# Kernel tuning notes

Measured on AMD Instinct MI355X. Metric: run time of the kernel, lower is better.

Reference implementation:

```python
import jax, jax.numpy as jnp
import numpy as np

B, T, V, E, H1, H2 = 256, 512, 50000, 300, 50, 10


def _lstm(xs, mask, W_ih, W_hh, b, hidden):
    """Masked LSTM over time-major xs [T,B,D]. mask [T,B,1]: True = valid step.
    Matches PyTorch gate order (i,f,g,o). Padded steps freeze (h,c), which is
    equivalent to pack_padded_sequence semantics (final hidden = state at last
    valid timestep)."""
    Bn = xs.shape[1]
    h0 = jnp.zeros((Bn, hidden), xs.dtype)
    c0 = jnp.zeros((Bn, hidden), xs.dtype)

    def step(carry, inp):
        h, c = carry
        x_t, m_t = inp
        g = x_t @ W_ih.T + h @ W_hh.T + b  # [B, 4H]
        i, f, gg, o = jnp.split(g, 4, axis=-1)
        c_new = jax.nn.sigmoid(f) * c + jax.nn.sigmoid(i) * jnp.tanh(gg)
        h_new = jax.nn.sigmoid(o) * jnp.tanh(c_new)
        h = jnp.where(m_t, h_new, h)
        c = jnp.where(m_t, c_new, c)
        return (h, c), h

    (hT, _), hs = jax.lax.scan(step, (h0, c0), (xs, mask))
    return hs, hT


def setup_inputs() -> dict:
    key = jax.random.key(0)
    ks = jax.random.split(key, 12)
    x = jax.random.randint(ks[0], (B, T), 0, V, dtype=jnp.int64)
    lengths = jax.random.randint(ks[1], (B,), 1, T + 1, dtype=jnp.int64)
    emb = jax.random.normal(ks[2], (V, E), dtype=jnp.float32)
    s1 = 1.0 / np.sqrt(H1)
    s2 = 1.0 / np.sqrt(H2)
    return {
        "x": x,
        "lengths": lengths,
        "emb": emb,
        "W_ih1": jax.random.uniform(ks[3], (4 * H1, E), jnp.float32, -s1, s1),
        "W_hh1": jax.random.uniform(ks[4], (4 * H1, H1), jnp.float32, -s1, s1),
        "b1": jax.random.uniform(ks[5], (4 * H1,), jnp.float32, -s1, s1),
        "W_ih2": jax.random.uniform(ks[6], (4 * H2, H1), jnp.float32, -s2, s2),
        "W_hh2": jax.random.uniform(ks[7], (4 * H2, H2), jnp.float32, -s2, s2),
        "b2": jax.random.uniform(ks[8], (4 * H2,), jnp.float32, -s2, s2),
        "fc1_w": jax.random.uniform(ks[9], (10, H2), jnp.float32, -s2, s2),
        "fc1_b": jnp.zeros((10,), jnp.float32),
        "fc2_w": jax.random.uniform(ks[10], (1, 10), jnp.float32, -s2, s2),
        "fc2_b": jnp.zeros((1,), jnp.float32),
    }


def reference(x, lengths, emb, W_ih1, W_hh1, b1, W_ih2, W_hh2, b2,
              fc1_w, fc1_b, fc2_w, fc2_b):
    e = emb[x]                                   # [B,T,E]
    xs = jnp.transpose(e, (1, 0, 2))             # time-major [T,B,E]
    mask = (jnp.arange(T)[:, None] < lengths[None, :])[..., None]  # [T,B,1]
    hs1, _ = _lstm(xs, mask, W_ih1, W_hh1, b1, H1)   # [T,B,50]
    _, h2 = _lstm(hs1, mask, W_ih2, W_hh2, b2, H2)   # final hidden [B,10]
    # dropout layers are identity in eval mode
    z = jax.nn.relu(h2 @ fc1_w.T + fc1_b)
    return z @ fc2_w.T + fc2_b                   # [B,1]
```

## Files before the change

### kernel.cpp

```cpp
#include <hip/hip_runtime.h>
#include <hip/hip_bf16.h>

#define BB 256
#define TT 512
#define EE 300
#define G4 200
#define NPAD 208
#define KP 1216
#define KC 64
#define KPD (KP/2)
#define KCD (KC/2)
#define NCH 19
#define NT 13
#define BOFF 8192
#define BUFB 34816

typedef __attribute__((ext_vector_type(8))) short short8v;
typedef __attribute__((ext_vector_type(4))) float float4v;
typedef __attribute__((ext_vector_type(4))) unsigned int uint4v;


__device__ __forceinline__ float sigm(float x) {
    return __builtin_amdgcn_rcpf(1.f + __builtin_amdgcn_exp2f(-1.442695040888963f * x));
}
__device__ __forceinline__ float tanh_(float x) {
    float t = __builtin_amdgcn_exp2f(2.885390081777927f * x);
    return 1.f - 2.f * __builtin_amdgcn_rcpf(t + 1.f);
}
template <int C>
__device__ __forceinline__ float qb(float v) {
    return __int_as_float(__builtin_amdgcn_mov_dpp(__float_as_int(v), C, 0xF, 0xF, true));
}

__device__ __forceinline__ uint2 bfsplit(float a) {
    unsigned u = __float_as_uint(a);
    unsigned rh = (u + 0x7FFFu + ((u >> 16) & 1u)) & 0xFFFF0000u;
    float l = a - __uint_as_float(rh);
    unsigned v = __float_as_uint(l);
    unsigned rl = (v + 0x7FFFu + ((v >> 16) & 1u)) >> 16;
    return make_uint2(rh >> 16, rl);
}

__global__ void wtrans_kernel(const float* __restrict__ W, const float* __restrict__ b1,
                              unsigned* __restrict__ Btg, float* __restrict__ b1p) {
    int e = blockIdx.x;
    int j = threadIdx.x;
    if (j >= NPAD) return;
    float w = 0.f;
    if (j < G4) w = W[((j & 3) * 50 + (j >> 2)) * EE + e];
    uint2 s = bfsplit(w);
    *(uint2*)(Btg + (size_t)j * KPD + 2 * e) =
        make_uint2(s.x | (s.x << 16), s.y | (s.y << 16));
    if (e == 0) b1p[j] = (j < G4) ? b1[(j & 3) * 50 + (j >> 2)] : 0.f;
}

__global__ __launch_bounds__(256, 2) void proj_kernel(
    const int* __restrict__ x, const int* __restrict__ lengths,
    const float* __restrict__ emb, const unsigned* __restrict__ Btg,
    const float* __restrict__ b1p, float* __restrict__ G1, int b0)
{
    const int b  = b0 + blockIdx.y;
    const int t0 = blockIdx.x * 64;
    const int len = lengths[b];
    if (t0 >= len) return;

    const int tid  = threadIdx.x;
    const int wv   = tid >> 6;
    const int lane = tid & 63;

    __shared__ __align__(16) char lds[2 * BUFB];

    const int arow = tid >> 2;
    const int ag   = tid & 3;
    const float* er = emb + (size_t)x[b * TT + t0 + arow] * EE;

    float4v acc[NT] = {};

    auto stageB = [&](int c, int q) {
        char* base = lds + q * BUFB + BOFF;
        #pragma unroll
        for (int rr = 0; rr < 7; ++rr) {
            if (rr < 6 || tid < 128) {
                int g   = rr * 256 + tid;
                int row = g >> 3, sl = g & 7;
                const unsigned* src = Btg + (size_t)row * KPD + c * KCD
                                      + ((sl ^ (row & 7)) << 2);
                char* dst = base + (rr * 256 + (tid & ~63)) * 16;
                __builtin_amdgcn_global_load_lds(
                    (const __attribute__((address_space(1))) void*)src,
                    (__attribute__((address_space(3))) void*)dst, 16, 0, 0);
            }
        }
    };
    auto loadA = [&](int cc) -> float4 {
        int k0 = cc * 16 + ag * 4;
        if (k0 < EE) return *(const float4*)(er + k0);
        return make_float4(0.f, 0.f, 0.f, 0.f);
    };
    auto writeA = [&](int q, float4 av) {
        uint2 s0 = bfsplit(av.x), s1 = bfsplit(av.y);
        uint2 s2 = bfsplit(av.z), s3 = bfsplit(av.w);
        unsigned p0 = s0.x | (s0.y << 16), p1 = s1.x | (s1.y << 16);
        unsigned p2 = s2.x | (s2.y << 16), p3 = s3.x | (s3.y << 16);
        char* base = lds + q * BUFB + (arow << 7);
        int r7 = arow & 7;
        *(uint4v*)(base + ((( 2 * ag    ) ^ r7) << 4)) = uint4v{p0, p0, p1, p1};
        *(uint4v*)(base + (((2 * ag + 1) ^ r7) << 4)) = uint4v{p2, p2, p3, p3};
    };

    stageB(0, 0);
    float4 aval = loadA(0);
    asm volatile("s_waitcnt vmcnt(0)" ::: "memory");
    writeA(0, aval);
    asm volatile("s_waitcnt lgkmcnt(0)" ::: "memory");
    __builtin_amdgcn_s_barrier();
    __builtin_amdgcn_sched_barrier(0);

    int p = 0;
    for (int c = 0; c < NCH; ++c) {
        const int q = p ^ 1;
        if (c + 1 < NCH) {
            stageB(c + 1, q);
            aval = loadA(c + 1);
        }
        const int r  = lane & 15;
        const int h  = lane >> 4;
        #pragma unroll
        for (int s = 0; s < 2; ++s) {
            const int sw4 = (((4 * s + h) ^ (r & 7)) << 4);
            short8v aF = *(const short8v*)(lds + p * BUFB + ((wv * 16 + r) << 7) + sw4);
            #pragma unroll
            for (int nt = 0; nt < NT; ++nt) {
                short8v bF = *(const short8v*)(lds + p * BUFB + BOFF
                                               + ((nt * 16 + r) << 7) + sw4);
                acc[nt] = __builtin_amdgcn_mfma_f32_16x16x32_bf16(aF, bF, acc[nt], 0, 0, 0);
            }
        }
        if (c + 1 < NCH) {
            asm volatile("s_waitcnt vmcnt(0)" ::: "memory");
            writeA(q, aval);
            asm volatile("s_waitcnt lgkmcnt(0)" ::: "memory");
            __builtin_amdgcn_s_barrier();
            __builtin_amdgcn_sched_barrier(0);
        }
        p = q;
    }

    float* gbase = G1 + ((size_t)blockIdx.y * TT + t0) * G4;
    const int col = lane & 15, rq = lane >> 4;
    #pragma unroll
    for (int nt = 0; nt < NT; ++nt) {
        int jp = nt * 16 + col;
        if (jp < G4) {
            float bias = b1p[jp];
            #pragma unroll
            for (int rr = 0; rr < 4; ++rr)
                gbase[(size_t)(wv * 16 + rq * 4 + rr) * G4 + jp] = acc[nt][rr] + bias;
        }
    }
}

__global__ __launch_bounds__(256, 1) void lstm_kernel(
    const int* __restrict__ lengths,
    const float* __restrict__ W_hh1, const float* __restrict__ W_ih2,
    const float* __restrict__ W_hh2, const float* __restrict__ b2,
    const float* __restrict__ fc1w, const float* __restrict__ fc1b,
    const float* __restrict__ fc2w, const float* __restrict__ fc2b,
    const float* __restrict__ G1, float* __restrict__ out, int b0)
{
    const int bb  = blockIdx.x;
    const int b   = b0 + bb;
    const int tid = threadIdx.x;
    const int len = lengths[b];

    __shared__ __align__(16) float hs[2][64];
    __shared__ __align__(16) float hfin[12];
    __shared__ float zbuf[10];

    if (tid < 64) { hs[0][tid] = 0.f; hs[1][tid] = 0.f; }

    const bool isL1 = (tid < 200);
    const bool isL2 = (tid >= 200 && tid < 240);

    float wreg[52];
    float wregb[12];
    #pragma unroll
    for (int k = 0; k < 52; ++k) wreg[k] = 0.f;
    #pragma unroll
    for (int k = 0; k < 12; ++k) wregb[k] = 0.f;
    float base2 = 0.f;

    if (isL1) {
        int u = tid >> 2, g = tid & 3;
        const float* wp = W_hh1 + (g * 50 + u) * 50;
        #pragma unroll
        for (int k = 0; k < 50; ++k) wreg[k] = wp[k];
    } else if (isL2) {
        int q = tid - 200, u = q >> 2, g = q & 3;
        int row = g * 10 + u;
        const float* wp = W_ih2 + row * 50;
        #pragma unroll
        for (int k = 0; k < 50; ++k) wreg[k] = wp[k];
        const float* wp2 = W_hh2 + row * 10;
        #pragma unroll
        for (int k = 0; k < 10; ++k) wregb[k] = wp2[k];
        base2 = b2[row];
    }

    const bool wr   = ((tid & 3) == 0) && (tid < 240);
    const int  slot = isL1 ? (tid >> 2) : (52 + ((tid - 200) >> 2));

    float h1v[52], h2v[12];
    #pragma unroll
    for (int k = 0; k < 52; ++k) h1v[k] = 0.f;
    #pragma unroll
    for (int k = 0; k < 12; ++k) h2v[k] = 0.f;

    float c = 0.f;
    const float* g1p = G1 + (size_t)bb * TT * G4;
    const int gcol = isL1 ? tid : 199;
    float g0, g1r, g2r;
    {
        int t1 = (1 < len) ? 1 : len - 1;
        int t2 = (2 < len) ? 2 : len - 1;
        g0  = g1p[gcol];
        g1r = g1p[(size_t)t1 * G4 + gcol];
        g2r = g1p[(size_t)t2 * G4 + gcol];
    }

    __syncthreads();

    for (int i = 0; i < len; ++i) {
        float base = isL1 ? g0 : base2;
        g0 = g1r; g1r = g2r;
        int tn = (i + 3 < len) ? i + 3 : len - 1;
        g2r = g1p[(size_t)tn * G4 + gcol];

        float s0 = 0.f, s1 = 0.f, s2 = 0.f, s3 = 0.f;
        #pragma unroll
        for (int m = 0; m < 13; ++m) {
            s0 = fmaf(wreg[4*m+0], h1v[4*m+0], s0);
            s1 = fmaf(wreg[4*m+1], h1v[4*m+1], s1);
            s2 = fmaf(wreg[4*m+2], h1v[4*m+2], s2);
            s3 = fmaf(wreg[4*m+3], h1v[4*m+3], s3);
        }
        #pragma unroll
        for (int m = 0; m < 3; ++m) {
            s0 = fmaf(wregb[4*m+0], h2v[4*m+0], s0);
            s1 = fmaf(wregb[4*m+1], h2v[4*m+1], s1);
            s2 = fmaf(wregb[4*m+2], h2v[4*m+2], s2);
            s3 = fmaf(wregb[4*m+3], h2v[4*m+3], s3);
        }
        float gv = base + (s0 + s1) + (s2 + s3);

        float gi = qb<0x00>(gv);
        float gf = qb<0x55>(gv);
        float gg = qb<0xAA>(gv);
        float go = qb<0xFF>(gv);
        float cn = sigm(gf) * c + sigm(gi) * tanh_(gg);
        float hn = sigm(go) * tanh_(cn);
        if (isL2 && i == 0) { cn = 0.f; hn = 0.f; }
        c = cn;
        if (wr) hs[i & 1][slot] = hn;

        asm volatile("s_waitcnt lgkmcnt(0)" ::: "memory");
        __builtin_amdgcn_s_barrier();
        __builtin_amdgcn_sched_barrier(0);

        const float* hb = hs[i & 1];
        #pragma unroll
        for (int m = 0; m < 13; ++m) {
            float4 v = *(const float4*)(hb + 4 * m);
            h1v[4*m+0] = v.x; h1v[4*m+1] = v.y;
            h1v[4*m+2] = v.z; h1v[4*m+3] = v.w;
        }
        if (tid >= 192) {
            #pragma unroll
            for (int m = 0; m < 3; ++m) {
                float4 v = *(const float4*)(hb + 52 + 4 * m);
                h2v[4*m+0] = v.x; h2v[4*m+1] = v.y;
                h2v[4*m+2] = v.z; h2v[4*m+3] = v.w;
            }
        }
    }

    if (isL2) {
        float s0 = 0.f, s1 = 0.f, s2 = 0.f, s3 = 0.f;
        #pragma unroll
        for (int m = 0; m < 13; ++m) {
            s0 = fmaf(wreg[4*m+0], h1v[4*m+0], s0);
            s1 = fmaf(wreg[4*m+1], h1v[4*m+1], s1);
            s2 = fmaf(wreg[4*m+2], h1v[4*m+2], s2);
            s3 = fmaf(wreg[4*m+3], h1v[4*m+3], s3);
        }
        #pragma unroll
        for (int m = 0; m < 3; ++m) {
            s0 = fmaf(wregb[4*m+0], h2v[4*m+0], s0);
            s1 = fmaf(wregb[4*m+1], h2v[4*m+1], s1);
            s2 = fmaf(wregb[4*m+2], h2v[4*m+2], s2);
            s3 = fmaf(wregb[4*m+3], h2v[4*m+3], s3);
        }
        float gv = base2 + (s0 + s1) + (s2 + s3);
        float gi = qb<0x00>(gv);
        float gf = qb<0x55>(gv);
        float gg = qb<0xAA>(gv);
        float go = qb<0xFF>(gv);
        float cn = sigm(gf) * c + sigm(gi) * tanh_(gg);
        float hn = sigm(go) * tanh_(cn);
        if ((tid & 3) == 0) hfin[(tid - 200) >> 2] = hn;
    }
    __syncthreads();

    if (tid < 10) {
        float s = fc1b[tid];
        #pragma unroll
        for (int e = 0; e < 10; ++e) s = fmaf(fc1w[tid * 10 + e], hfin[e], s);
        zbuf[tid] = s > 0.f ? s : 0.f;
    }
    __syncthreads();
    if (tid == 0) {
        float s = fc2b[0];
        #pragma unroll
        for (int e = 0; e < 10; ++e) s = fmaf(fc2w[e], zbuf[e], s);
        out[b] = s;
    }
}

extern "C" void kernel_launch(void* const* d_in, const int* in_sizes, int n_in,
                              void* d_out, int out_size, void* d_ws, size_t ws_size,
                              hipStream_t stream)
{
    const int*   x     = (const int*)  d_in[0];
    const int*   len   = (const int*)  d_in[1];
    const float* emb   = (const float*)d_in[2];
    const float* W_ih1 = (const float*)d_in[3];
    const float* W_hh1 = (const float*)d_in[4];
    const float* b1    = (const float*)d_in[5];
    const float* W_ih2 = (const float*)d_in[6];
    const float* W_hh2 = (const float*)d_in[7];
    const float* b2    = (const float*)d_in[8];
    const float* fc1w  = (const float*)d_in[9];
    const float* fc1b  = (const float*)d_in[10];
    const float* fc2w  = (const float*)d_in[11];
    const float* fc2b  = (const float*)d_in[12];
    float* out = (float*)d_out;

    const size_t btg_bytes = (size_t)NPAD * KPD * sizeof(unsigned);
    const size_t b1p_off = btg_bytes;
    const size_t head = (b1p_off + NPAD * sizeof(float) + 255) & ~255ull;
    const size_t per_b = (size_t)TT * G4 * sizeof(float);

    unsigned* Btg = (unsigned*)d_ws;
    float*    b1p = (float*)((char*)d_ws + b1p_off);
    float*    G1  = (float*)((char*)d_ws + head);

    size_t avail = ws_size > head ? ws_size - head : 0;
    int chunk = (int)(avail / per_b);
    if (chunk < 1) chunk = 1;
    if (chunk > BB) chunk = BB;

    wtrans_kernel<<<dim3(EE), dim3(256), 0, stream>>>(W_ih1, b1, Btg, b1p);

    for (int b0 = 0; b0 < BB; b0 += chunk) {
        int nb = (BB - b0) < chunk ? (BB - b0) : chunk;
        proj_kernel<<<dim3(TT / 64, nb), dim3(256), 0, stream>>>(
            x, len, emb, Btg, b1p, G1, b0);
        lstm_kernel<<<dim3(nb), dim3(256), 0, stream>>>(
            len, W_hh1, W_ih2, W_hh2, b2, fc1w, fc1b, fc2w, fc2b, G1, out, b0);
    }
}
```

Baseline: 347.7 us.

## Pack two batch elements per LSTM workgroup and fold final layer-2 step into loop

Each LSTM workgroup now runs two batch sequences with 512 threads, so 128 blocks are launched instead of 256. Per-element masking freezes state once that element's length is reached. The loop runs to the pair's maximum length plus one, which folds in the trailing layer-2 step that used to follow the loop. The intent is to raise per-CU occupancy and hide barrier and latency costs, since 256 single-wave-group blocks were latency bound. The cost is that the shorter sequence of each pair idles until the longer one finishes, and barriers now span 8 waves.

```diff
diff --git a/kernel.cpp b/kernel.cpp
--- a/kernel.cpp
+++ b/kernel.cpp
@@ -160,27 +160,33 @@
     }
 }
 
-__global__ __launch_bounds__(256, 1) void lstm_kernel(
+__global__ __launch_bounds__(512, 1) void lstm_kernel(
     const int* __restrict__ lengths,
     const float* __restrict__ W_hh1, const float* __restrict__ W_ih2,
     const float* __restrict__ W_hh2, const float* __restrict__ b2,
     const float* __restrict__ fc1w, const float* __restrict__ fc1b,
     const float* __restrict__ fc2w, const float* __restrict__ fc2b,
-    const float* __restrict__ G1, float* __restrict__ out, int b0)
+    const float* __restrict__ G1, float* __restrict__ out, int b0, int nb)
 {
-    const int bb  = blockIdx.x;
-    const int b   = b0 + bb;
     const int tid = threadIdx.x;
-    const int len = lengths[b];
-
-    __shared__ __align__(16) float hs[2][64];
-    __shared__ __align__(16) float hfin[12];
-    __shared__ float zbuf[10];
-
-    if (tid < 64) { hs[0][tid] = 0.f; hs[1][tid] = 0.f; }
-
-    const bool isL1 = (tid < 200);
-    const bool isL2 = (tid >= 200 && tid < 240);
+    const int e   = tid >> 8;
+    const int et  = tid & 255;
+
+    const int last = b0 + nb - 1;
+    const int eg0  = b0 + blockIdx.x * 2;
+    int eg = eg0 + e;       if (eg > last) eg = last;
+    int egB = eg0 + 1;      if (egB > last) egB = last;
+    const int len    = lengths[eg];
+    const int lenmax = max(lengths[eg0], lengths[egB]);
+
+    __shared__ __align__(16) float hs[2][2][64];
+    __shared__ __align__(16) float hfin[2][12];
+    __shared__ float zbuf[2][10];
+
+    if (et < 64) { hs[e][0][et] = 0.f; hs[e][1][et] = 0.f; }
+
+    const bool isL1 = (et < 200);
+    const bool isL2 = (et >= 200 && et < 240);
 
     float wreg[52];
     float wregb[12];
@@ -191,12 +197,12 @@
     float base2 = 0.f;
 
     if (isL1) {
-        int u = tid >> 2, g = tid & 3;
+        int u = et >> 2, g = et & 3;
         const float* wp = W_hh1 + (g * 50 + u) * 50;
         #pragma unroll
         for (int k = 0; k < 50; ++k) wreg[k] = wp[k];
     } else if (isL2) {
-        int q = tid - 200, u = q >> 2, g = q & 3;
+        int q = et - 200, u = q >> 2, g = q & 3;
         int row = g * 10 + u;
         const float* wp = W_ih2 + row * 50;
         #pragma unroll
@@ -207,8 +213,8 @@
         base2 = b2[row];
     }
 
-    const bool wr   = ((tid & 3) == 0) && (tid < 240);
-    const int  slot = isL1 ? (tid >> 2) : (52 + ((tid - 200) >> 2));
+    const bool wr   = ((et & 3) == 0) && (et < 240);
+    const int  slot = isL1 ? (et >> 2) : (52 + ((et - 200) >> 2));
 
     float h1v[52], h2v[12];
     #pragma unroll
@@ -216,9 +222,9 @@
     #pragma unroll
     for (int k = 0; k < 12; ++k) h2v[k] = 0.f;
 
-    float c = 0.f;
-    const float* g1p = G1 + (size_t)bb * TT * G4;
-    const int gcol = isL1 ? tid : 199;
+    float c = 0.f, hkeep = 0.f;
+    const float* g1p = G1 + (size_t)(eg - b0) * TT * G4;
+    const int gcol = isL1 ? et : 199;
     float g0, g1r, g2r;
     {
         int t1 = (1 < len) ? 1 : len - 1;
@@ -230,7 +236,7 @@
 
     __syncthreads();
 
-    for (int i = 0; i < len; ++i) {
+    for (int i = 0; i <= lenmax; ++i) {
         float base = isL1 ? g0 : base2;
         g0 = g1r; g1r = g2r;
         int tn = (i + 3 < len) ? i + 3 : len - 1;
@@ -259,22 +265,24 @@
         float go = qb<0xFF>(gv);
         float cn = sigm(gf) * c + sigm(gi) * tanh_(gg);
         float hn = sigm(go) * tanh_(cn);
-        if (isL2 && i == 0) { cn = 0.f; hn = 0.f; }
-        c = cn;
-        if (wr) hs[i & 1][slot] = hn;
+
+        bool upd = isL1 ? (i < len) : (i >= 1 && i <= len);
+        c = upd ? cn : c;
+        hkeep = upd ? hn : hkeep;
+        if (wr) hs[e][i & 1][slot] = hkeep;
 
         asm volatile("s_waitcnt lgkmcnt(0)" ::: "memory");
         __builtin_amdgcn_s_barrier();
         __builtin_amdgcn_sched_barrier(0);
 
-        const float* hb = hs[i & 1];
+        const float* hb = hs[e][i & 1];
         #pragma unroll
         for (int m = 0; m < 13; ++m) {
             float4 v = *(const float4*)(hb + 4 * m);
             h1v[4*m+0] = v.x; h1v[4*m+1] = v.y;
             h1v[4*m+2] = v.z; h1v[4*m+3] = v.w;
         }
-        if (tid >= 192) {
+        if (et >= 192) {
             #pragma unroll
             for (int m = 0; m < 3; ++m) {
                 float4 v = *(const float4*)(hb + 52 + 4 * m);
@@ -284,45 +292,21 @@
         }
     }
 
-    if (isL2) {
-        float s0 = 0.f, s1 = 0.f, s2 = 0.f, s3 = 0.f;
-        #pragma unroll
-        for (int m = 0; m < 13; ++m) {
-            s0 = fmaf(wreg[4*m+0], h1v[4*m+0], s0);
-            s1 = fmaf(wreg[4*m+1], h1v[4*m+1], s1);
-            s2 = fmaf(wreg[4*m+2], h1v[4*m+2], s2);
-            s3 = fmaf(wreg[4*m+3], h1v[4*m+3], s3);
-        }
-        #pragma unroll
-        for (int m = 0; m < 3; ++m) {
-            s0 = fmaf(wregb[4*m+0], h2v[4*m+0], s0);
-            s1 = fmaf(wregb[4*m+1], h2v[4*m+1], s1);
-            s2 = fmaf(wregb[4*m+2], h2v[4*m+2], s2);
-            s3 = fmaf(wregb[4*m+3], h2v[4*m+3], s3);
-        }
-        float gv = base2 + (s0 + s1) + (s2 + s3);
-        float gi = qb<0x00>(gv);
-        float gf = qb<0x55>(gv);
-        float gg = qb<0xAA>(gv);
-        float go = qb<0xFF>(gv);
-        float cn = sigm(gf) * c + sigm(gi) * tanh_(gg);
-        float hn = sigm(go) * tanh_(cn);
-        if ((tid & 3) == 0) hfin[(tid - 200) >> 2] = hn;
-    }
+    if (isL2 && (et & 3) == 0) hfin[e][(et - 200) >> 2] = hkeep;
     __syncthreads();
 
-    if (tid < 10) {
-        float s = fc1b[tid];
-        #pragma unroll
-        for (int e = 0; e < 10; ++e) s = fmaf(fc1w[tid * 10 + e], hfin[e], s);
-        zbuf[tid] = s > 0.f ? s : 0.f;
+    if (et < 10) {
+        float s = fc1b[et];
+        #pragma unroll
+        for (int k = 0; k < 10; ++k) s = fmaf(fc1w[et * 10 + k], hfin[e][k], s);
+        zbuf[e][et] = s > 0.f ? s : 0.f;
     }
     __syncthreads();
-    if (tid == 0) {
+    if (et == 0) {
         float s = fc2b[0];
         #pragma unroll
-        for (int e = 0; e < 10; ++e) s = fmaf(fc2w[e], zbuf[e], s);
-        out[b] = s;
+        for (int k = 0; k < 10; ++k) s = fmaf(fc2w[k], zbuf[e][k], s);
+        out[eg] = s;
     }
 }
 
@@ -356,7 +340,7 @@
 
     size_t avail = ws_size > head ? ws_size - head : 0;
     int chunk = (int)(avail / per_b);
-    if (chunk < 1) chunk = 1;
+    if (chunk < 2) chunk = 2;
     if (chunk > BB) chunk = BB;
 
     wtrans_kernel<<<dim3(EE), dim3(256), 0, stream>>>(W_ih1, b1, Btg, b1p);
@@ -365,7 +349,7 @@
         int nb = (BB - b0) < chunk ? (BB - b0) : chunk;
         proj_kernel<<<dim3(TT / 64, nb), dim3(256), 0, stream>>>(
             x, len, emb, Btg, b1p, G1, b0);
-        lstm_kernel<<<dim3(nb), dim3(256), 0, stream>>>(
-            len, W_hh1, W_ih2, W_hh2, b2, fc1w, fc1b, fc2w, fc2b, G1, out, b0);
-    }
-}
+        lstm_kernel<<<dim3((nb + 1) / 2), dim3(512), 0, stream>>>(
+            len, W_hh1, W_ih2, W_hh2, b2, fc1w, fc1b, fc2w, fc2b, G1, out, b0, nb);
+    }
+}
```

New measurement: 441.4 us. 1.27x slower.

## Run recurrent LSTM in a single wavefront per sequence without barriers

Applied to the files above, without the earlier changes.

Shrinks the recurrent kernel from 256 threads to one 64-lane wavefront per batch row. Each lane now computes all four gates of one hidden unit, so the DPP gate exchange and the workgroup barrier are gone; lanes exchange h through LDS using only lgkmcnt waits. The cost is four times more FMAs per lane, 256 weight registers per lane, and reliance on wavefront lockstep for LDS ordering.

```diff
diff --git a/kernel.cpp b/kernel.cpp
--- a/kernel.cpp
+++ b/kernel.cpp
@@ -26,10 +26,6 @@
 __device__ __forceinline__ float tanh_(float x) {
     float t = __builtin_amdgcn_exp2f(2.885390081777927f * x);
     return 1.f - 2.f * __builtin_amdgcn_rcpf(t + 1.f);
-}
-template <int C>
-__device__ __forceinline__ float qb(float v) {
-    return __int_as_float(__builtin_amdgcn_mov_dpp(__float_as_int(v), C, 0xF, 0xF, true));
 }
 
 __device__ __forceinline__ uint2 bfsplit(float a) {
@@ -160,7 +156,7 @@
     }
 }
 
-__global__ __launch_bounds__(256, 1) void lstm_kernel(
+__global__ __launch_bounds__(64, 1) void lstm_kernel(
     const int* __restrict__ lengths,
     const float* __restrict__ W_hh1, const float* __restrict__ W_ih2,
     const float* __restrict__ W_hh2, const float* __restrict__ b2,
@@ -168,160 +164,157 @@
     const float* __restrict__ fc2w, const float* __restrict__ fc2b,
     const float* __restrict__ G1, float* __restrict__ out, int b0)
 {
-    const int bb  = blockIdx.x;
-    const int b   = b0 + bb;
-    const int tid = threadIdx.x;
+    const int bb = blockIdx.x;
+    const int b  = b0 + bb;
+    const int u  = threadIdx.x;
     const int len = lengths[b];
 
     __shared__ __align__(16) float hs[2][64];
-    __shared__ __align__(16) float hfin[12];
-    __shared__ float zbuf[10];
-
-    if (tid < 64) { hs[0][tid] = 0.f; hs[1][tid] = 0.f; }
-
-    const bool isL1 = (tid < 200);
-    const bool isL2 = (tid >= 200 && tid < 240);
-
-    float wreg[52];
-    float wregb[12];
+    __shared__ float hfin[12];
+    __shared__ float zbuf[12];
+
+    hs[0][u] = 0.f;
+    hs[1][u] = 0.f;
+
+    const bool isL1 = (u < 50);
+    const bool isL2 = (u >= 50 && u < 60);
+
+    float4 w[4][16];
     #pragma unroll
-    for (int k = 0; k < 52; ++k) wreg[k] = 0.f;
-    #pragma unroll
-    for (int k = 0; k < 12; ++k) wregb[k] = 0.f;
-    float base2 = 0.f;
+    for (int g = 0; g < 4; ++g)
+        #pragma unroll
+        for (int m = 0; m < 16; ++m)
+            w[g][m] = make_float4(0.f, 0.f, 0.f, 0.f);
 
     if (isL1) {
-        int u = tid >> 2, g = tid & 3;
-        const float* wp = W_hh1 + (g * 50 + u) * 50;
-        #pragma unroll
-        for (int k = 0; k < 50; ++k) wreg[k] = wp[k];
+        #pragma unroll
+        for (int g = 0; g < 4; ++g) {
+            const float* wp = W_hh1 + (g * 50 + u) * 50;
+            #pragma unroll
+            for (int m = 0; m < 12; ++m)
+                w[g][m] = make_float4(wp[4*m], wp[4*m+1], wp[4*m+2], wp[4*m+3]);
+            w[g][12].x = wp[48];
+            w[g][12].y = wp[49];
+        }
     } else if (isL2) {
-        int q = tid - 200, u = q >> 2, g = q & 3;
-        int row = g * 10 + u;
-        const float* wp = W_ih2 + row * 50;
-        #pragma unroll
-        for (int k = 0; k < 50; ++k) wreg[k] = wp[k];
-        const float* wp2 = W_hh2 + row * 10;
-        #pragma unroll
-        for (int k = 0; k < 10; ++k) wregb[k] = wp2[k];
-        base2 = b2[row];
-    }
-
-    const bool wr   = ((tid & 3) == 0) && (tid < 240);
-    const int  slot = isL1 ? (tid >> 2) : (52 + ((tid - 200) >> 2));
-
-    float h1v[52], h2v[12];
-    #pragma unroll
-    for (int k = 0; k < 52; ++k) h1v[k] = 0.f;
-    #pragma unroll
-    for (int k = 0; k < 12; ++k) h2v[k] = 0.f;
-
-    float c = 0.f;
-    const float* g1p = G1 + (size_t)bb * TT * G4;
-    const int gcol = isL1 ? tid : 199;
-    float g0, g1r, g2r;
+        #pragma unroll
+        for (int g = 0; g < 4; ++g) {
+            int row = g * 10 + (u - 50);
+            const float* wp = W_ih2 + row * 50;
+            #pragma unroll
+            for (int m = 0; m < 12; ++m)
+                w[g][m] = make_float4(wp[4*m], wp[4*m+1], wp[4*m+2], wp[4*m+3]);
+            w[g][12].x = wp[48];
+            w[g][12].y = wp[49];
+            const float* wq = W_hh2 + row * 10;
+            w[g][13] = make_float4(wq[0], wq[1], wq[2], wq[3]);
+            w[g][14] = make_float4(wq[4], wq[5], wq[6], wq[7]);
+            w[g][15].x = wq[8];
+            w[g][15].y = wq[9];
+        }
+    }
+
+    float4 bb4 = make_float4(0.f, 0.f, 0.f, 0.f);
+    if (isL2) {
+        int u2 = u - 50;
+        bb4 = make_float4(b2[u2], b2[10 + u2], b2[20 + u2], b2[30 + u2]);
+    }
+
+    const float* g1p = G1 + (size_t)bb * TT * G4 + (isL1 ? 4 * u : 0);
+    float4 f0, f1, f2;
     {
         int t1 = (1 < len) ? 1 : len - 1;
         int t2 = (2 < len) ? 2 : len - 1;
-        g0  = g1p[gcol];
-        g1r = g1p[(size_t)t1 * G4 + gcol];
-        g2r = g1p[(size_t)t2 * G4 + gcol];
-    }
-
-    __syncthreads();
+        f0 = *(const float4*)(g1p);
+        f1 = *(const float4*)(g1p + (size_t)t1 * G4);
+        f2 = *(const float4*)(g1p + (size_t)t2 * G4);
+    }
+
+    const int  slot = isL1 ? u : (52 + (u - 50));
+    const bool wr   = (u < 60);
+
+    float c = 0.f, hkeep = 0.f;
+    asm volatile("s_waitcnt lgkmcnt(0)" ::: "memory");
 
     for (int i = 0; i < len; ++i) {
-        float base = isL1 ? g0 : base2;
-        g0 = g1r; g1r = g2r;
+        float4 gb = isL1 ? f0 : bb4;
+        f0 = f1; f1 = f2;
         int tn = (i + 3 < len) ? i + 3 : len - 1;
-        g2r = g1p[(size_t)tn * G4 + gcol];
-
-        float s0 = 0.f, s1 = 0.f, s2 = 0.f, s3 = 0.f;
-        #pragma unroll
-        for (int m = 0; m < 13; ++m) {
-            s0 = fmaf(wreg[4*m+0], h1v[4*m+0], s0);
-            s1 = fmaf(wreg[4*m+1], h1v[4*m+1], s1);
-            s2 = fmaf(wreg[4*m+2], h1v[4*m+2], s2);
-            s3 = fmaf(wreg[4*m+3], h1v[4*m+3], s3);
-        }
-        #pragma unroll
-        for (int m = 0; m < 3; ++m) {
-            s0 = fmaf(wregb[4*m+0], h2v[4*m+0], s0);
-            s1 = fmaf(wregb[4*m+1], h2v[4*m+1], s1);
-            s2 = fmaf(wregb[4*m+2], h2v[4*m+2], s2);
-            s3 = fmaf(wregb[4*m+3], h2v[4*m+3], s3);
-        }
-        float gv = base + (s0 + s1) + (s2 + s3);
-
-        float gi = qb<0x00>(gv);
-        float gf = qb<0x55>(gv);
-        float gg = qb<0xAA>(gv);
-        float go = qb<0xFF>(gv);
-        float cn = sigm(gf) * c + sigm(gi) * tanh_(gg);
-        float hn = sigm(go) * tanh_(cn);
+        f2 = *(const float4*)(g1p + (size_t)tn * G4);
+
+        float a0 = gb.x, a1 = gb.y, a2 = gb.z, a3 = gb.w;
+        const float* hb = hs[i & 1];
+        #pragma unroll
+        for (int m = 0; m < 16; ++m) {
+            float4 hv = *(const float4*)(hb + 4 * m);
+            a0 = fmaf(w[0][m].x, hv.x, a0);
+            a1 = fmaf(w[1][m].x, hv.x, a1);
+            a2 = fmaf(w[2][m].x, hv.x, a2);
+            a3 = fmaf(w[3][m].x, hv.x, a3);
+            a0 = fmaf(w[0][m].y, hv.y, a0);
+            a1 = fmaf(w[1][m].y, hv.y, a1);
+            a2 = fmaf(w[2][m].y, hv.y, a2);
+            a3 = fmaf(w[3][m].y, hv.y, a3);
+            a0 = fmaf(w[0][m].z, hv.z, a0);
+            a1 = fmaf(w[1][m].z, hv.z, a1);
+            a2 = fmaf(w[2][m].z, hv.z, a2);
+            a3 = fmaf(w[3][m].z, hv.z, a3);
+            a0 = fmaf(w[0][m].w, hv.w, a0);
+            a1 = fmaf(w[1][m].w, hv.w, a1);
+            a2 = fmaf(w[2][m].w, hv.w, a2);
+            a3 = fmaf(w[3][m].w, hv.w, a3);
+        }
+
+        float cn = sigm(a1) * c + sigm(a0) * tanh_(a2);
+        float hn = sigm(a3) * tanh_(cn);
         if (isL2 && i == 0) { cn = 0.f; hn = 0.f; }
         c = cn;
-        if (wr) hs[i & 1][slot] = hn;
+        hkeep = hn;
+        if (wr) hs[(i & 1) ^ 1][slot] = hn;
 
         asm volatile("s_waitcnt lgkmcnt(0)" ::: "memory");
-        __builtin_amdgcn_s_barrier();
-        __builtin_amdgcn_sched_barrier(0);
-
-        const float* hb = hs[i & 1];
-        #pragma unroll
-        for (int m = 0; m < 13; ++m) {
-            float4 v = *(const float4*)(hb + 4 * m);
-            h1v[4*m+0] = v.x; h1v[4*m+1] = v.y;
-            h1v[4*m+2] = v.z; h1v[4*m+3] = v.w;
-        }
-        if (tid >= 192) {
-            #pragma unroll
-            for (int m = 0; m < 3; ++m) {
-                float4 v = *(const float4*)(hb + 52 + 4 * m);
-                h2v[4*m+0] = v.x; h2v[4*m+1] = v.y;
-                h2v[4*m+2] = v.z; h2v[4*m+3] = v.w;
-            }
-        }
-    }
-
-    if (isL2) {
-        float s0 = 0.f, s1 = 0.f, s2 = 0.f, s3 = 0.f;
-        #pragma unroll
-        for (int m = 0; m < 13; ++m) {
-            s0 = fmaf(wreg[4*m+0], h1v[4*m+0], s0);
-            s1 = fmaf(wreg[4*m+1], h1v[4*m+1], s1);
-            s2 = fmaf(wreg[4*m+2], h1v[4*m+2], s2);
-            s3 = fmaf(wreg[4*m+3], h1v[4*m+3], s3);
-        }
-        #pragma unroll
-        for (int m = 0; m < 3; ++m) {
-            s0 = fmaf(wregb[4*m+0], h2v[4*m+0], s0);
-            s1 = fmaf(wregb[4*m+1], h2v[4*m+1], s1);
-            s2 = fmaf(wregb[4*m+2], h2v[4*m+2], s2);
-            s3 = fmaf(wregb[4*m+3], h2v[4*m+3], s3);
-        }
-        float gv = base2 + (s0 + s1) + (s2 + s3);
-        float gi = qb<0x00>(gv);
-        float gf = qb<0x55>(gv);
-        float gg = qb<0xAA>(gv);
-        float go = qb<0xFF>(gv);
-        float cn = sigm(gf) * c + sigm(gi) * tanh_(gg);
-        float hn = sigm(go) * tanh_(cn);
-        if ((tid & 3) == 0) hfin[(tid - 200) >> 2] = hn;
-    }
-    __syncthreads();
-
-    if (tid < 10) {
-        float s = fc1b[tid];
-        #pragma unroll
-        for (int e = 0; e < 10; ++e) s = fmaf(fc1w[tid * 10 + e], hfin[e], s);
-        zbuf[tid] = s > 0.f ? s : 0.f;
-    }
-    __syncthreads();
-    if (tid == 0) {
+    }
+
+    {
+        float a0 = bb4.x, a1 = bb4.y, a2 = bb4.z, a3 = bb4.w;
+        const float* hb = hs[len & 1];
+        #pragma unroll
+        for (int m = 0; m < 16; ++m) {
+            float4 hv = *(const float4*)(hb + 4 * m);
+            a0 = fmaf(w[0][m].x, hv.x, a0);
+            a1 = fmaf(w[1][m].x, hv.x, a1);
+            a2 = fmaf(w[2][m].x, hv.x, a2);
+            a3 = fmaf(w[3][m].x, hv.x, a3);
+            a0 = fmaf(w[0][m].y, hv.y, a0);
+            a1 = fmaf(w[1][m].y, hv.y, a1);
+            a2 = fmaf(w[2][m].y, hv.y, a2);
+            a3 = fmaf(w[3][m].y, hv.y, a3);
+            a0 = fmaf(w[0][m].z, hv.z, a0);
+            a1 = fmaf(w[1][m].z, hv.z, a1);
+            a2 = fmaf(w[2][m].z, hv.z, a2);
+            a3 = fmaf(w[3][m].z, hv.z, a3);
+            a0 = fmaf(w[0][m].w, hv.w, a0);
+            a1 = fmaf(w[1][m].w, hv.w, a1);
+            a2 = fmaf(w[2][m].w, hv.w, a2);
+            a3 = fmaf(w[3][m].w, hv.w, a3);
+        }
+        float cn = sigm(a1) * c + sigm(a0) * tanh_(a2);
+        float hn = sigm(a3) * tanh_(cn);
+        if (isL2) hfin[u - 50] = hn;
+    }
+    asm volatile("s_waitcnt lgkmcnt(0)" ::: "memory");
+
+    if (u < 10) {
+        float s = fc1b[u];
+        #pragma unroll
+        for (int k = 0; k < 10; ++k) s = fmaf(fc1w[u * 10 + k], hfin[k], s);
+        zbuf[u] = s > 0.f ? s : 0.f;
+    }
+    asm volatile("s_waitcnt lgkmcnt(0)" ::: "memory");
+    if (u == 0) {
         float s = fc2b[0];
         #pragma unroll
-        for (int e = 0; e < 10; ++e) s = fmaf(fc2w[e], zbuf[e], s);
+        for (int k = 0; k < 10; ++k) s = fmaf(fc2w[k], zbuf[k], s);
         out[b] = s;
     }
 }
@@ -365,7 +358,7 @@
         int nb = (BB - b0) < chunk ? (BB - b0) : chunk;
         proj_kernel<<<dim3(TT / 64, nb), dim3(256), 0, stream>>>(
             x, len, emb, Btg, b1p, G1, b0);
-        lstm_kernel<<<dim3(nb), dim3(256), 0, stream>>>(
+        lstm_kernel<<<dim3(nb), dim3(64), 0, stream>>>(
             len, W_hh1, W_ih2, W_hh2, b2, fc1w, fc1b, fc2w, fc2b, G1, out, b0);
     }
 }
```

Measured after the change: 543.0 us. 56.1% more time.
